# Kernel tuning notes

Measured on AMD Instinct MI355X. Metric: run time of the kernel, lower is better.

The kernel has to match this reference:

```python
import jax, jax.numpy as jnp
import numpy as np

NUM_STEPS = 10
NUM_NODES = 100000
NUM_EDGES = 6400000


def setup_inputs() -> dict:
    key = jax.random.key(0)
    k1, k2, k3 = jax.random.split(key, 3)
    x = jax.random.uniform(k1, (NUM_NODES, 1), dtype=jnp.float32)
    edge_index = jax.random.randint(k2, (2, NUM_EDGES), 0, NUM_NODES, dtype=jnp.int64)
    edge_probs = jax.random.uniform(k3, (NUM_EDGES,), dtype=jnp.float32)
    # learned parameters (match torch init)
    time_decay = jnp.linspace(0.0, 1.0, NUM_STEPS, dtype=jnp.float32)
    node_bias = jnp.float32(0.0)
    edge_weight = jnp.ones((NUM_STEPS,), dtype=jnp.float32)
    return {
        "x": x,
        "edge_index": edge_index,
        "edge_probs": edge_probs,
        "time_decay": time_decay,
        "node_bias": node_bias,
        "edge_weight": edge_weight,
    }


def reference(x, edge_index, edge_probs, time_decay, node_bias, edge_weight):
    src, dst = edge_index[0], edge_index[1]
    num_nodes = x.shape[0]
    # per-step scalar scale: edge_weight[i] * exp(-time_decay[i]^2)
    step_scale = edge_weight * jnp.exp(-(time_decay ** 2))  # (num_steps,)

    def step(carry, scale):
        cur, surv = carry
        # gather node state to edges, scale, scatter-add back to nodes
        messages = cur[src] * (edge_probs[:, None] * scale)  # (num_edges, 1)
        cur = jax.ops.segment_sum(messages, dst, num_segments=num_nodes)
        cur = cur + node_bias
        surv = surv * (1.0 - cur)
        return (cur, surv), None

    (_, survival_prob), _ = jax.lax.scan(step, (x, 1.0 - x), step_scale)
    final_infection = 1.0 - survival_prob
    return jnp.clip(final_infection, 0.0, 1.0)
```

## Files before the change

### kernel.cpp

```cpp
#include <hip/hip_runtime.h>
#include <math.h>


#define MAXBINS     64
#define BIN_SHIFT   11
#define BIN_SIZE    2048
#define STAGE_CAP   64
#define BUCKET_GRID 1024
#define BUCKET_TPB  256
#define BUCKET_K    8
#define STEP_TPB    1024

__global__ void k_detect(const unsigned long long* ei, int* flag) {
    if (blockIdx.x == 0 && threadIdx.x == 0) {
        int is64 = 1;
        for (int k = 0; k < 64; ++k)
            if ((ei[k] >> 32) != 0ULL) { is64 = 0; break; }
        *flag = is64;
    }
}

__global__ void k_scales(const float* __restrict__ time_decay,
                         const float* __restrict__ edge_weight,
                         float* __restrict__ step_scale, int num_steps,
                         unsigned int* __restrict__ gcur) {
    int i = threadIdx.x;
    if (i < num_steps) {
        float td = time_decay[i];
        step_scale[i] = edge_weight[i] * expf(-td * td);
    }
    if (i < MAXBINS) gcur[i] = 0u;
}

__global__ void k_init(const float* __restrict__ x, float* __restrict__ cur0,
                       float* __restrict__ surv, int n) {
    int i = blockIdx.x * blockDim.x + threadIdx.x;
    if (i < n) {
        float v = x[i];
        cur0[i] = v;
        surv[i] = 1.0f - v;
    }
}

__global__ void k_bucket(const void* __restrict__ ei_raw, const int* __restrict__ flag,
                         const float* __restrict__ probs, unsigned int* __restrict__ gcur,
                         float2* __restrict__ sorted, unsigned int capr,
                         int E, int nbins) {
    __shared__ float2 buf[MAXBINS][STAGE_CAP];
    __shared__ unsigned int cnt[MAXBINS];
    __shared__ unsigned int gbase[MAXBINS];
    const int t = threadIdx.x;
    const int wid = t >> 6, lane = t & 63;
    const int nwaves = BUCKET_TPB / 64;
    const int is64 = *flag;
    const int chunk = (E + gridDim.x - 1) / gridDim.x;
    const int beg = blockIdx.x * chunk;
    const int end = min(E, beg + chunk);
    for (int i = t; i < nbins; i += BUCKET_TPB) cnt[i] = 0u;
    __syncthreads();
    const int ROUND = BUCKET_TPB * BUCKET_K;
    for (int rbeg = beg; rbeg < end; rbeg += ROUND) {
        for (int k = 0; k < BUCKET_K; ++k) {
            int e = rbeg + k * BUCKET_TPB + t;
            if (e < end) {
                int src, dst;
                if (is64) {
                    const long long* s = (const long long*)ei_raw;
                    src = (int)s[e]; dst = (int)s[e + E];
                } else {
                    const int* s = (const int*)ei_raw;
                    src = s[e]; dst = s[e + E];
                }
                float pr = probs[e];
                int bin = dst >> BIN_SHIFT;
                unsigned int payload = (unsigned int)src |
                                       ((unsigned int)(dst & (BIN_SIZE - 1)) << 17);
                unsigned int pos = atomicAdd(&cnt[bin], 1u);
                if (pos < STAGE_CAP) {
                    buf[bin][pos] = make_float2(__uint_as_float(payload), pr);
                } else {
                    unsigned int gp = atomicAdd(&gcur[bin], 1u);
                    if (gp < capr)
                        sorted[(size_t)bin * capr + gp] =
                            make_float2(__uint_as_float(payload), pr);
                }
            }
        }
        __syncthreads();
        if (t < nbins) {
            unsigned int c = min(cnt[t], (unsigned int)STAGE_CAP);
            if (c > 0u) gbase[t] = atomicAdd(&gcur[t], c);
        }
        __syncthreads();
        for (int b = wid; b < nbins; b += nwaves) {
            unsigned int c = min(cnt[b], (unsigned int)STAGE_CAP);
            if ((unsigned int)lane < c) {
                unsigned int gp = gbase[b] + (unsigned int)lane;
                if (gp < capr)
                    sorted[(size_t)b * capr + gp] = buf[b][lane];
            }
        }
        __syncthreads();
        for (int i = t; i < nbins; i += BUCKET_TPB) cnt[i] = 0u;
        __syncthreads();
    }
}

__global__ void __launch_bounds__(STEP_TPB)
k_step(const float2* __restrict__ sorted, const unsigned int* __restrict__ gcur,
       const float* __restrict__ cur_in, float* __restrict__ part,
       unsigned int capr, int pstride, int nbins, int splits) {
    __shared__ float acc[4][BIN_SIZE];
    const int bin = blockIdx.x / splits;
    const int sp  = blockIdx.x - bin * splits;
    const int t = threadIdx.x;
    float* accf = (float*)acc;
    for (int i = t; i < 4 * BIN_SIZE; i += STEP_TPB) accf[i] = 0.0f;
    __syncthreads();
    unsigned int cntv = min(gcur[bin], capr);
    unsigned int sub = (cntv + (unsigned int)splits - 1) / (unsigned int)splits;
    unsigned int s0 = min(cntv, (unsigned int)sp * sub);
    unsigned int s1 = min(cntv, s0 + sub);
    const float2* base = sorted + (size_t)bin * capr;
    for (unsigned int j = s0 + t; j < s1; j += STEP_TPB) {
        float2 kp = base[j];
        unsigned int v = __float_as_uint(kp.x);
        float m = cur_in[v & 0x1FFFFu] * kp.y;
        atomicAdd(&acc[t & 3][v >> 17], m);
    }
    __syncthreads();
    float* dst = part + (size_t)sp * pstride + (size_t)bin * BIN_SIZE;
    for (int i = t; i < BIN_SIZE; i += STEP_TPB)
        dst[i] = acc[0][i] + acc[1][i] + acc[2][i] + acc[3][i];
}

__global__ void k_reduce(const float* __restrict__ part, int pstride, int splits,
                         float* __restrict__ cur_out, float* __restrict__ surv,
                         const float* __restrict__ step_scale, const float* __restrict__ bias_p,
                         float* __restrict__ out, int step, int n, int last) {
    int i = blockIdx.x * blockDim.x + threadIdx.x;
    if (i >= n) return;
    float c = 0.0f;
    for (int s = 0; s < splits; ++s) c += part[(size_t)s * pstride + i];
    c = c * step_scale[step] + bias_p[0];
    if (!last) cur_out[i] = c;
    float sv = surv[i] * (1.0f - c);
    surv[i] = sv;
    if (last) out[i] = fminf(fmaxf(1.0f - sv, 0.0f), 1.0f);
}

__global__ void k_init0(const float* __restrict__ x, float* __restrict__ cur,
                        float* __restrict__ surv, float* __restrict__ acc, int n) {
    int i = blockIdx.x * blockDim.x + threadIdx.x;
    if (i < n) {
        float v = x[i];
        cur[i] = v; surv[i] = 1.0f - v; acc[i] = 0.0f;
    }
}

__global__ void k_edge_raw(const void* __restrict__ ei_raw, const int* __restrict__ flag,
                           const float* __restrict__ probs, const float* __restrict__ cur,
                           float* __restrict__ acc, const float* __restrict__ step_scale,
                           int step, int num_edges) {
    const float scale = step_scale[step];
    const int is64 = *flag;
    const int stride = gridDim.x * blockDim.x;
    for (int e = blockIdx.x * blockDim.x + threadIdx.x; e < num_edges; e += stride) {
        int src, dst;
        if (is64) {
            const long long* s = (const long long*)ei_raw;
            src = (int)s[e]; dst = (int)s[e + num_edges];
        } else {
            const int* s = (const int*)ei_raw;
            src = s[e]; dst = s[e + num_edges];
        }
        atomicAdd(&acc[dst], cur[src] * (probs[e] * scale));
    }
}

__global__ void k_node(float* __restrict__ cur, float* __restrict__ acc,
                       float* __restrict__ surv, const float* __restrict__ bias_p,
                       float* __restrict__ out, int n, int write_out) {
    int i = blockIdx.x * blockDim.x + threadIdx.x;
    if (i < n) {
        float c = acc[i] + bias_p[0];
        acc[i] = 0.0f;
        cur[i] = c;
        float s = surv[i] * (1.0f - c);
        surv[i] = s;
        if (write_out) out[i] = fminf(fmaxf(1.0f - s, 0.0f), 1.0f);
    }
}

static inline size_t al256(size_t x) { return (x + 255) & ~(size_t)255; }

extern "C" void kernel_launch(void* const* d_in, const int* in_sizes, int n_in,
                              void* d_out, int out_size, void* d_ws, size_t ws_size,
                              hipStream_t stream) {
    const float* x           = (const float*)d_in[0];
    const void*  ei          = d_in[1];
    const float* probs       = (const float*)d_in[2];
    const float* time_decay  = (const float*)d_in[3];
    const float* node_bias   = (const float*)d_in[4];
    const float* edge_weight = (const float*)d_in[5];
    float* outf = (float*)d_out;

    const int n = in_sizes[0];
    const int E = in_sizes[2];
    const int S = in_sizes[3];

    char* ws = (char*)d_ws;
    int*          flag       = (int*)ws;
    float*        step_scale = (float*)(ws + 64);
    unsigned int* gcur       = (unsigned int*)(ws + 256);

    const int nbins   = (n + BIN_SIZE - 1) >> BIN_SHIFT;
    const int pstride = nbins * BIN_SIZE;

    const double   meand  = (double)E / (nbins > 0 ? nbins : 1);
    const double   sigma  = sqrt(meand > 1.0 ? meand : 1.0);
    unsigned int   want   = (unsigned int)(meand + 16.0 * sigma + 64.0);
    unsigned int   least  = (unsigned int)(meand + 6.0 * sigma + 64.0);
    want  = (want  + 63u) & ~63u;
    least = (least + 63u) & ~63u;

    const size_t nbA      = al256((size_t)n * 4);
    const size_t off_buf  = 512;
    const size_t off_surv = off_buf + nbA;
    const size_t off_part = al256(off_surv + nbA);

    int splits = 0;
    unsigned int capr = 0;
    size_t off_sort = 0;
    const int cand[4] = {8, 6, 5, 4};
    for (int ci = 0; ci < 4; ++ci) {
        int sp = cand[ci];
        size_t part_b = (size_t)sp * pstride * 4;
        size_t osort  = al256(off_part + part_b);
        if (ws_size <= osort) continue;
        size_t availb = ws_size - osort;
        unsigned int acap = (unsigned int)((availb / ((size_t)nbins * 8)) & ~(size_t)63);
        if (acap >= least) {
            splits  = sp;
            capr    = acap < want ? acap : want;
            off_sort = osort;
            break;
        }
    }

    const int nthreads  = 256;
    const int node_grid = (n + nthreads - 1) / nthreads;

    const bool ok = (n <= (1 << 17)) && (nbins >= 1) && (nbins <= MAXBINS) &&
                    (E > 0) && (splits > 0);

    k_detect<<<1, 64, 0, stream>>>((const unsigned long long*)ei, flag);
    k_scales<<<1, 64, 0, stream>>>(time_decay, edge_weight, step_scale, S, gcur);

    if (!ok) {
        float* cur  = (float*)(ws + off_buf);
        float* surv = (float*)(ws + off_surv);
        float* acc  = (float*)(ws + off_surv + nbA);
        k_init0<<<node_grid, nthreads, 0, stream>>>(x, cur, surv, acc, n);
        for (int s = 0; s < S; ++s) {
            k_edge_raw<<<2048, nthreads, 0, stream>>>(ei, flag, probs, cur, acc,
                                                      step_scale, s, E);
            k_node<<<node_grid, nthreads, 0, stream>>>(cur, acc, surv, node_bias,
                                                       outf, n, s == S - 1 ? 1 : 0);
        }
        return;
    }

    float*  bufA   = (float*)(ws + off_buf);
    float*  surv   = (float*)(ws + off_surv);
    float*  part   = (float*)(ws + off_part);
    float2* sorted = (float2*)(ws + off_sort);

    float* b0 = (S % 2 == 0) ? outf : bufA;
    float* b1 = (S % 2 == 0) ? bufA : outf;

    k_init<<<node_grid, nthreads, 0, stream>>>(x, b0, surv, n);

    k_bucket<<<BUCKET_GRID, BUCKET_TPB, 0, stream>>>(ei, flag, probs, gcur, sorted,
                                                     capr, E, nbins);

    const int step_grid = nbins * splits;
    for (int s = 0; s < S; ++s) {
        float* ci = (s % 2 == 0) ? b0 : b1;
        float* co = (s % 2 == 0) ? b1 : b0;
        k_step<<<step_grid, STEP_TPB, 0, stream>>>(sorted, gcur, ci, part,
                                                   capr, pstride, nbins, splits);
        k_reduce<<<node_grid, nthreads, 0, stream>>>(part, pstride, splits, co, surv,
                                                     step_scale, node_bias, outf,
                                                     s, n, s == S - 1 ? 1 : 0);
    }
}
```

Baseline: 682.0 us.

## Vectorize step-kernel edge loads, shrink blocks, raise split count

The per-step scatter kernel now runs 256-thread blocks with a single shared accumulator instead of four replicas. Each thread reads four packed edges with two 16-byte loads, and the per-split ranges are rounded up to multiples of four. The split candidates rise from 4–8 to 8–40, giving many more blocks per bin so the GPU is better filled. In exchange, more shared-atomic contention falls on one copy of the bin, and the larger partial buffer makes the reduce kernel read more data.

```diff
diff --git a/kernel.cpp b/kernel.cpp
--- a/kernel.cpp
+++ b/kernel.cpp
@@ -9,7 +9,7 @@
 #define BUCKET_GRID 1024
 #define BUCKET_TPB  256
 #define BUCKET_K    8
-#define STEP_TPB    1024
+#define STEP_TPB    256
 
 __global__ void k_detect(const unsigned long long* ei, int* flag) {
     if (blockIdx.x == 0 && threadIdx.x == 0) {
@@ -110,28 +110,43 @@
 k_step(const float2* __restrict__ sorted, const unsigned int* __restrict__ gcur,
        const float* __restrict__ cur_in, float* __restrict__ part,
        unsigned int capr, int pstride, int nbins, int splits) {
-    __shared__ float acc[4][BIN_SIZE];
+    __shared__ float acc[BIN_SIZE];
     const int bin = blockIdx.x / splits;
     const int sp  = blockIdx.x - bin * splits;
     const int t = threadIdx.x;
-    float* accf = (float*)acc;
-    for (int i = t; i < 4 * BIN_SIZE; i += STEP_TPB) accf[i] = 0.0f;
+    for (int i = t; i < BIN_SIZE; i += STEP_TPB) acc[i] = 0.0f;
     __syncthreads();
     unsigned int cntv = min(gcur[bin], capr);
-    unsigned int sub = (cntv + (unsigned int)splits - 1) / (unsigned int)splits;
+    unsigned int sub = ((cntv + (unsigned int)splits - 1) / (unsigned int)splits + 3u) & ~3u;
     unsigned int s0 = min(cntv, (unsigned int)sp * sub);
     unsigned int s1 = min(cntv, s0 + sub);
     const float2* base = sorted + (size_t)bin * capr;
-    for (unsigned int j = s0 + t; j < s1; j += STEP_TPB) {
-        float2 kp = base[j];
-        unsigned int v = __float_as_uint(kp.x);
-        float m = cur_in[v & 0x1FFFFu] * kp.y;
-        atomicAdd(&acc[t & 3][v >> 17], m);
+    for (unsigned int j = s0 + (unsigned int)t * 4u; j < s1; j += STEP_TPB * 4u) {
+        if (j + 4u <= s1) {
+            float4 a = *reinterpret_cast<const float4*>(base + j);
+            float4 b = *reinterpret_cast<const float4*>(base + j + 2);
+            unsigned int k0 = __float_as_uint(a.x), k1 = __float_as_uint(a.z);
+            unsigned int k2 = __float_as_uint(b.x), k3 = __float_as_uint(b.z);
+            float m0 = cur_in[k0 & 0x1FFFFu] * a.y;
+            float m1 = cur_in[k1 & 0x1FFFFu] * a.w;
+            float m2 = cur_in[k2 & 0x1FFFFu] * b.y;
+            float m3 = cur_in[k3 & 0x1FFFFu] * b.w;
+            atomicAdd(&acc[k0 >> 17], m0);
+            atomicAdd(&acc[k1 >> 17], m1);
+            atomicAdd(&acc[k2 >> 17], m2);
+            atomicAdd(&acc[k3 >> 17], m3);
+        } else {
+            for (unsigned int q = j; q < s1; ++q) {
+                float2 kp = base[q];
+                unsigned int k = __float_as_uint(kp.x);
+                atomicAdd(&acc[k >> 17], cur_in[k & 0x1FFFFu] * kp.y);
+            }
+        }
     }
     __syncthreads();
     float* dst = part + (size_t)sp * pstride + (size_t)bin * BIN_SIZE;
     for (int i = t; i < BIN_SIZE; i += STEP_TPB)
-        dst[i] = acc[0][i] + acc[1][i] + acc[2][i] + acc[3][i];
+        dst[i] = acc[i];
 }
 
 __global__ void k_reduce(const float* __restrict__ part, int pstride, int splits,
@@ -232,8 +247,8 @@
     int splits = 0;
     unsigned int capr = 0;
     size_t off_sort = 0;
-    const int cand[4] = {8, 6, 5, 4};
-    for (int ci = 0; ci < 4; ++ci) {
+    const int cand[5] = {40, 32, 24, 16, 8};
+    for (int ci = 0; ci < 5; ++ci) {
         int sp = cand[ci];
         size_t part_b = (size_t)sp * pstride * 4;
         size_t osort  = al256(off_part + part_b);
```

New measurement: 695.6 us. About the same (+2.0%).
